# Kernel optimization log

Measured on AMD Instinct MI355X. Metric: run time of the kernel, lower is better.

## Reference

```python
import jax, jax.numpy as jnp
import numpy as np

B, S, DIM = 4, 2048, 1024
HEADS, HD = 16, DIM // 16
HIDDEN, LEVELS = 4 * DIM, 3
LN_EPS = 1e-5


def setup_inputs() -> dict:
    key = jax.random.key(0)
    ks = jax.random.split(key, 10)
    w = lambda k, shape: (jax.random.normal(k, shape, jnp.float32) * 0.02)
    return {
        "x": jax.random.normal(ks[0], (B, S, DIM), jnp.float32),
        "Wq": w(ks[1], (DIM, DIM)),
        "Wk": w(ks[2], (DIM, DIM)),
        "Wv": w(ks[3], (DIM, DIM)),
        "Wo": w(ks[4], (DIM, DIM)),
        "ln1_g": jnp.ones((DIM,), jnp.float32),
        "ln1_b": jnp.zeros((DIM,), jnp.float32),
        "ln2_g": jnp.ones((DIM,), jnp.float32),
        "ln2_b": jnp.zeros((DIM,), jnp.float32),
        "cms_w1": w(ks[5], (LEVELS, DIM, HIDDEN)),
        "cms_b1": jnp.zeros((LEVELS, HIDDEN), jnp.float32),
        "cms_w2": w(ks[6], (LEVELS, HIDDEN, DIM)),
        "cms_b2": jnp.zeros((LEVELS, DIM), jnp.float32),
    }


def _layer_norm(x, g, b):
    m = jnp.mean(x, axis=-1, keepdims=True)
    v = jnp.var(x, axis=-1, keepdims=True)
    return (x - m) * jax.lax.rsqrt(v + LN_EPS) * g + b


def _linear_attn(h, Wq, Wk, Wv, Wo):
    # h: [B, S, DIM]; feature_map(z) = elu(z) + 1 applied to Q and K
    fm = lambda z: jax.nn.elu(z) + 1.0
    Q = fm(h @ Wq).reshape(B, S, HEADS, HD)
    K = fm(h @ Wk).reshape(B, S, HEADS, HD)
    V = (h @ Wv).reshape(B, S, HEADS, HD)
    # scan over time with fast-weight memory M_t = M_{t-1} + k_t (x) v_t
    Qs = jnp.moveaxis(Q, 1, 0)  # [S, B, H, D]
    Ks = jnp.moveaxis(K, 1, 0)
    Vs = jnp.moveaxis(V, 1, 0)

    def step(carry, qkv):
        mem, ksum = carry  # [B,H,D,D], [B,H,D]
        q, k, v = qkv      # each [B,H,D]
        mem = mem + k[..., :, None] * v[..., None, :]
        ksum = ksum + k
        num = jnp.einsum('bhde,bhd->bhe', mem, q)
        den = jnp.einsum('bhd,bhd->bh', ksum, q)[..., None] + 1e-6
        return (mem, ksum), num / den

    init = (jnp.zeros((B, HEADS, HD, HD), h.dtype),
            jnp.zeros((B, HEADS, HD), h.dtype))
    _, ys = jax.lax.scan(step, init, (Qs, Ks, Vs))  # ys: [S,B,H,D]
    out = jnp.moveaxis(ys, 0, 1).reshape(B, S, DIM)
    return out @ Wo


def _cms(h, w1, b1, w2, b2):
    # Continuum Memory System: chain of LEVELS MLPs (dim->4dim->dim).
    y = h
    for l in range(LEVELS):
        y = jax.nn.gelu(y @ w1[l] + b1[l]) @ w2[l] + b2[l]
    return y


def reference(x, Wq, Wk, Wv, Wo, ln1_g, ln1_b, ln2_g, ln2_b,
              cms_w1, cms_b1, cms_w2, cms_b2):
    x = x + _linear_attn(_layer_norm(x, ln1_g, ln1_b), Wq, Wk, Wv, Wo)
    x = x + _cms(_layer_norm(x, ln2_g, ln2_b), cms_w1, cms_b1, cms_w2, cms_b2)
    return x
```

## Files before the change

kernel.cpp:

```cpp
#include <hip/hip_runtime.h>
#include <stdint.h>
#include <math.h>

#define DIM     1024
#define HID     4096
#define SEQ     2048
#define NB      4
#define NH      16
#define HD      64
#define NCHUNK  32
#define MROWS   8192
#define QSTR    3072

typedef unsigned short ushort_t;
typedef __attribute__((ext_vector_type(8))) short bf16x8;
typedef __attribute__((ext_vector_type(4))) float f32x4;

#define OFF_H    ((size_t)0)
#define OFF_Q    ((size_t)16777216)
#define OFF_P    ((size_t)67108864)
#define OFF_KS   ((size_t)100663296)
#define OFF_X1   ((size_t)101187584)
#define OFF_WQT  ((size_t)134742016)
#define OFF_WOT  ((size_t)141033472)
#define OFF_W1T  ((size_t)143130624)
#define OFF_W2T  ((size_t)168296448)
#define OFF_HIDB OFF_Q + 16777216

__device__ __forceinline__ float b2f(ushort_t u) {
    return __uint_as_float(((unsigned int)u) << 16);
}
__device__ __forceinline__ ushort_t f2b(float f) {
    unsigned int u = __float_as_uint(f);
    u += 0x7FFFu + ((u >> 16) & 1u);
    return (ushort_t)(u >> 16);
}
__device__ __forceinline__ void unpack4(uint2 u, float* f) {
    f[0] = __uint_as_float(u.x << 16);
    f[1] = __uint_as_float(u.x & 0xffff0000u);
    f[2] = __uint_as_float(u.y << 16);
    f[3] = __uint_as_float(u.y & 0xffff0000u);
}
__device__ __forceinline__ float fast_gelu(float x) {
    const float u = x * (1.5957691216057308f + 0.07135481627f * x * x);
    const float e = exp2f(-1.4426950408889634f * u);
    return x * __builtin_amdgcn_rcpf(1.0f + e);
}
__device__ __forceinline__ float fast_elu1(float x) {
    return x > 0.0f ? x + 1.0f : exp2f(1.4426950408889634f * x);
}
__device__ __forceinline__ void ldg16(const ushort_t* g, ushort_t* l) {
    __builtin_amdgcn_global_load_lds(
        (const __attribute__((address_space(1))) void*)g,
        (__attribute__((address_space(3))) void*)l, 16, 0, 0);
}

__global__ void __launch_bounds__(256)
transpose_f32_bf16(const float* __restrict__ src, ushort_t* __restrict__ dst, int R, int C)
{
    __shared__ float t[32][33];
    const int bx = blockIdx.x * 32;
    const int by = blockIdx.y * 32;
    const int tx = threadIdx.x, ty = threadIdx.y;
    #pragma unroll
    for (int i = ty; i < 32; i += 8)
        t[i][tx] = src[(size_t)(by + i) * C + bx + tx];
    __syncthreads();
    #pragma unroll
    for (int i = ty; i < 32; i += 8)
        dst[(size_t)(bx + i) * R + by + tx] = f2b(t[tx][i]);
}

__global__ void __launch_bounds__(256)
ln_fwd(const float* __restrict__ xin, const float* __restrict__ g,
       const float* __restrict__ be, ushort_t* __restrict__ out)
{
    const int row = blockIdx.x, tid = threadIdx.x;
    const float4 f = ((const float4*)(xin + (size_t)row * DIM))[tid];
    float v[4] = {f.x, f.y, f.z, f.w};
    float s  = v[0] + v[1] + v[2] + v[3];
    float ss = v[0]*v[0] + v[1]*v[1] + v[2]*v[2] + v[3]*v[3];
    #pragma unroll
    for (int off = 32; off; off >>= 1) {
        s  += __shfl_down(s, off);
        ss += __shfl_down(ss, off);
    }
    __shared__ float red[2][4];
    const int wave = tid >> 6, lane = tid & 63;
    if (lane == 0) { red[0][wave] = s; red[1][wave] = ss; }
    __syncthreads();
    s  = red[0][0] + red[0][1] + red[0][2] + red[0][3];
    ss = red[1][0] + red[1][1] + red[1][2] + red[1][3];
    const float mean = s * (1.0f / DIM);
    const float var  = ss * (1.0f / DIM) - mean * mean;
    const float rstd = rsqrtf(var + 1e-5f);
    ushort_t o[4];
    #pragma unroll
    for (int i = 0; i < 4; i++) {
        const int col = tid * 4 + i;
        o[i] = f2b((v[i] - mean) * rstd * g[col] + be[col]);
    }
    uint2 u2;
    u2.x = (unsigned int)o[0] | ((unsigned int)o[1] << 16);
    u2.y = (unsigned int)o[2] | ((unsigned int)o[3] << 16);
    *(uint2*)(out + (size_t)row * DIM + tid * 4) = u2;
}

#define ACT_NONE 0
#define ACT_ELU1 1
#define ACT_GELU 2
#define ACT_QKV  3


#define G_RD_A(BUF, FR0) \
    _Pragma("unroll") for (int _i = 0; _i < 4; ++_i) \
    _Pragma("unroll") for (int _kk = 0; _kk < 2; ++_kk) \
        af[_i][_kk] = *(const bf16x8*)(ldsb + (BUF) + aoff + (((FR0) + _i) << 11) \
                                       + (((_kk << 6) | qv16) ^ mflip))

#define G_RD_B(BUF, F) \
    _Pragma("unroll") for (int _kk = 0; _kk < 2; ++_kk) \
        bf[(F)][_kk] = *(const bf16x8*)(ldsb + (BUF) + boff + ((F) << 13) \
                                        + (((_kk << 6) | qv16) ^ mflip))

#define G_MFMA(AR, C0, CNT) \
    _Pragma("unroll") for (int _i = 0; _i < 4; ++_i) \
    _Pragma("unroll") for (int _c = 0; _c < (CNT); ++_c) \
    _Pragma("unroll") for (int _kk = 0; _kk < 2; ++_kk) \
        acc[(AR) + _i][(C0) + _c] = __builtin_amdgcn_mfma_f32_16x16x32_bf16( \
            af[_i][_kk], bf[(C0) + _c][_kk], acc[(AR) + _i][(C0) + _c], 0, 0, 0)

#define ST_A(BUFO, T, R) ldg16(pA + (size_t)(R) * K + (size_t)(T) * 64, \
    (ushort_t*)(ldsb + (BUFO) + ((R) << 7) + (tid << 4)))
#define ST_B(BUFO, T, R) ldg16(pB + (size_t)(R) * K + (size_t)(T) * 64, \
    (ushort_t*)(ldsb + (BUFO) + 32768 + ((R) << 7) + (tid << 4)))

#define G_BARW() do { \
    __builtin_amdgcn_s_barrier(); \
    asm volatile("s_waitcnt lgkmcnt(0)" ::: "memory"); \
    __builtin_amdgcn_sched_barrier(0); \
    __builtin_amdgcn_s_setprio(1); \
} while (0)

#define G_ENDP() do { \
    __builtin_amdgcn_s_setprio(0); \
    __builtin_amdgcn_s_barrier(); \
} while (0)

#define G_TILE(BUFO, TS) do { \
     \
    G_RD_A(BUFO, 0); \
    _Pragma("unroll") for (int _f = 0; _f < NF / 2; ++_f) G_RD_B(BUFO, _f); \
    G_BARW(); G_MFMA(0, 0, NF / 2); G_ENDP(); \
     \
    _Pragma("unroll") for (int _f = NF / 2; _f < NF; ++_f) G_RD_B(BUFO, _f); \
    if (more) { ST_A(BUFO, TS, 0); ST_A(BUFO, TS, 128); ST_B(BUFO, TS, 0); } \
    G_BARW(); G_MFMA(0, NF / 2, NF / 2); G_ENDP(); \
     \
    G_RD_A(BUFO, 4); \
    if (more) { \
        ST_B(BUFO, TS, 64); \
        if constexpr (NF == 4) { ST_B(BUFO, TS, 128); ST_B(BUFO, TS, 192); } \
    } \
    G_BARW(); G_MFMA(4, 0, NF / 2); G_ENDP(); \
     \
    if (more) { ST_A(BUFO, TS, 64); ST_A(BUFO, TS, 192); } \
    G_BARW(); G_MFMA(4, NF / 2, NF / 2); \
    __builtin_amdgcn_s_setprio(0); \
    if (more) asm volatile("s_waitcnt vmcnt(%0)" :: "i"(LPT) : "memory"); \
    else      asm volatile("s_waitcnt vmcnt(0)" ::: "memory"); \
    __builtin_amdgcn_s_barrier(); \
} while (0)

template<int BN_, int ACT, bool BIAS, bool RES, bool OUTF32>
__global__ void __launch_bounds__(512, 2)
gemm256(const ushort_t* __restrict__ A, const ushort_t* __restrict__ Bt,
        const float* __restrict__ bias, const float* __restrict__ resid,
        void* __restrict__ Cout, int M, int N, int K)
{
    constexpr int NF    = BN_ / 64;
    constexpr int BUFSZ = 32768 + BN_ * 128;
    constexpr int LPT   = 4 + NF;
    __shared__ __align__(16) char ldsb[2 * BUFSZ];

    const int tid  = threadIdx.x;
    const int lane = tid & 63, wave = tid >> 6;
    const int wm_idx = wave >> 2, wn_idx = wave & 3;
    const int bm = blockIdx.x * 256, bn = blockIdx.y * BN_;

    const int r0  = tid >> 3;
    const int kbs = (((tid & 7) ^ (r0 & 7)) << 4);
    const ushort_t* pA = A  + (size_t)(bm + r0) * K + (kbs >> 1);
    const ushort_t* pB = Bt + (size_t)(bn + r0) * K + (kbs >> 1);

    const int m     = lane & 15;
    const int qv16  = (lane >> 4) << 4;
    const int mflip = (m & 7) << 4;
    const int aoff  = (wm_idx * 128 + m) << 7;
    const int boff  = 32768 + ((wn_idx * 16 + m) << 7);

    f32x4  acc[8][NF] = {};
    bf16x8 af[4][2], bf[NF][2];

    const int NT    = K >> 6;
    const int niter = NT >> 1;

    ST_A(0, 0, 0); ST_A(0, 0, 64); ST_A(0, 0, 128); ST_A(0, 0, 192);
    ST_B(0, 0, 0); ST_B(0, 0, 64);
    if constexpr (NF == 4) { ST_B(0, 0, 128); ST_B(0, 0, 192); }
    ST_A(BUFSZ, 1, 0); ST_A(BUFSZ, 1, 64); ST_A(BUFSZ, 1, 128); ST_A(BUFSZ, 1, 192);
    ST_B(BUFSZ, 1, 0); ST_B(BUFSZ, 1, 64);
    if constexpr (NF == 4) { ST_B(BUFSZ, 1, 128); ST_B(BUFSZ, 1, 192); }
    asm volatile("s_waitcnt vmcnt(%0)" :: "i"(LPT) : "memory");
    __builtin_amdgcn_s_barrier();

    for (int it = 0; it < niter; ++it) {
        const int  t    = it << 1;
        const bool more = (it + 1) < niter;
        G_TILE(0,     t + 2);
        G_TILE(BUFSZ, t + 3);
    }

    const int cr   = (lane >> 4) << 2;
    const int ccol = lane & 15;
    #pragma unroll
    for (int fr = 0; fr < 8; ++fr) {
        #pragma unroll
        for (int fc = 0; fc < NF; ++fc) {
            const int gc = bn + fc * 64 + wn_idx * 16 + ccol;
            const float bv = BIAS ? bias[gc] : 0.0f;
            #pragma unroll
            for (int j = 0; j < 4; ++j) {
                const int gr = bm + wm_idx * 128 + fr * 16 + cr + j;
                float vv = acc[fr][fc][j] + bv;
                if (ACT == ACT_ELU1) vv = fast_elu1(vv);
                if (ACT == ACT_GELU) vv = fast_gelu(vv);
                if (ACT == ACT_QKV)  vv = (bn < 2048) ? fast_elu1(vv) : vv;
                const size_t oidx = (size_t)gr * N + gc;
                if (RES) vv += resid[oidx];
                if (OUTF32) ((float*)Cout)[oidx] = vv;
                else        ((ushort_t*)Cout)[oidx] = f2b(vv);
            }
        }
    }
    (void)M;
}

__global__ void __launch_bounds__(256)
attn_phase1(const ushort_t* __restrict__ qkv,
            float* __restrict__ P, float* __restrict__ Ksum)
{
    const int c = blockIdx.x, h = blockIdx.y, b = blockIdx.z;
    __shared__ ushort_t Ks[64][68], Vs[64][68];
    const int tid = threadIdx.x;
    const size_t rowbase = (size_t)b * SEQ + c * 64;
    #pragma unroll
    for (int i = 0; i < 4; i++) {
        const int lin = tid + 256 * i;
        const int t = lin >> 4, d4 = (lin & 15) * 4;
        const size_t gidx = (rowbase + t) * QSTR + h * HD + d4;
        *(uint2*)&Ks[t][d4] = *(const uint2*)(qkv + 1024 + gidx);
        *(uint2*)&Vs[t][d4] = *(const uint2*)(qkv + 2048 + gidx);
    }
    __syncthreads();
    const int d0 = (tid >> 4) * 4, e0 = (tid & 15) * 4;
    float acc[4][4] = {};
    for (int t = 0; t < 64; t++) {
        float kf[4], vf[4];
        unpack4(*(const uint2*)&Ks[t][d0], kf);
        unpack4(*(const uint2*)&Vs[t][e0], vf);
        #pragma unroll
        for (int i = 0; i < 4; i++)
            #pragma unroll
            for (int j = 0; j < 4; j++)
                acc[i][j] += kf[i] * vf[j];
    }
    const size_t pbase = (((size_t)b * NH + h) * NCHUNK + c) * 4096;
    #pragma unroll
    for (int i = 0; i < 4; i++) {
        float4 o; o.x = acc[i][0]; o.y = acc[i][1]; o.z = acc[i][2]; o.w = acc[i][3];
        *(float4*)(P + pbase + (size_t)(d0 + i) * 64 + e0) = o;
    }
    if (tid < 64) {
        float a = 0.0f;
        for (int t = 0; t < 64; t++) a += b2f(Ks[t][tid]);
        Ksum[(((size_t)b * NH + h) * NCHUNK + c) * 64 + tid] = a;
    }
}

__global__ void __launch_bounds__(256)
attn_prefix(float* __restrict__ P, float* __restrict__ Ksum)
{
    const int bh = blockIdx.y;
    const int e  = blockIdx.x * 256 + threadIdx.x;
    const size_t base = (size_t)bh * NCHUNK * 4096 + e;
    float acc = 0.0f;
    #pragma unroll
    for (int c = 0; c < NCHUNK; c++) {
        const float t = P[base + (size_t)c * 4096];
        P[base + (size_t)c * 4096] = acc;
        acc += t;
    }
    if (blockIdx.x == 0 && threadIdx.x < 64) {
        const size_t kb = (size_t)bh * NCHUNK * 64 + threadIdx.x;
        float a = 0.0f;
        #pragma unroll
        for (int c = 0; c < NCHUNK; c++) {
            const float t = Ksum[kb + c * 64];
            Ksum[kb + c * 64] = a;
            a += t;
        }
    }
}

__global__ void __launch_bounds__(256)
attn_phase2(const ushort_t* __restrict__ qkv, const float* __restrict__ P,
            const float* __restrict__ Ksum, ushort_t* __restrict__ Out)
{
    const int c = blockIdx.x, h = blockIdx.y, b = blockIdx.z;
    const int tid = threadIdx.x;
    __shared__ ushort_t Qs[64][68], KsB[64][68], VsB[64][68];
    __shared__ float S[64][68];
    __shared__ float Mp[64][64];
    __shared__ float kp[64];
    __shared__ float partial[4][64];
    const size_t rowbase = (size_t)b * SEQ + c * 64;
    const size_t pbase = (((size_t)b * NH + h) * NCHUNK + c) * 4096;
    #pragma unroll
    for (int i = 0; i < 4; i++) {
        const int lin = tid + 256 * i;
        const int t = lin >> 4, d4 = (lin & 15) * 4;
        const size_t gidx = (rowbase + t) * QSTR + h * HD + d4;
        *(uint2*)&Qs[t][d4]  = *(const uint2*)(qkv + gidx);
        *(uint2*)&KsB[t][d4] = *(const uint2*)(qkv + 1024 + gidx);
        *(uint2*)&VsB[t][d4] = *(const uint2*)(qkv + 2048 + gidx);
        *(float4*)&Mp[t][d4] = *(const float4*)(P + pbase + lin * 4);
    }
    if (tid < 64) kp[tid] = Ksum[(((size_t)b * NH + h) * NCHUNK + c) * 64 + tid];
    __syncthreads();

    const int t0 = (tid >> 4) * 4;
    const int c0 = (tid & 15) * 4;

    {
        float accS[4][4] = {};
        for (int d4 = 0; d4 < 64; d4 += 4) {
            float qf[4][4], kf[4][4];
            #pragma unroll
            for (int i = 0; i < 4; i++) {
                unpack4(*(const uint2*)&Qs[t0 + i][d4], qf[i]);
                unpack4(*(const uint2*)&KsB[c0 + i][d4], kf[i]);
            }
            #pragma unroll
            for (int i = 0; i < 4; i++)
                #pragma unroll
                for (int j = 0; j < 4; j++)
                    #pragma unroll
                    for (int dd = 0; dd < 4; dd++)
                        accS[i][j] += qf[i][dd] * kf[j][dd];
        }
        #pragma unroll
        for (int i = 0; i < 4; i++) {
            float4 sv;
            sv.x = (c0 + 0 <= t0 + i) ? accS[i][0] : 0.0f;
            sv.y = (c0 + 1 <= t0 + i) ? accS[i][1] : 0.0f;
            sv.z = (c0 + 2 <= t0 + i) ? accS[i][2] : 0.0f;
            sv.w = (c0 + 3 <= t0 + i) ? accS[i][3] : 0.0f;
            *(float4*)&S[t0 + i][c0] = sv;
        }
    }
    __syncthreads();

    {
        const int t = tid & 63, q = tid >> 6;
        const int base = q * 16;
        float a = 0.0f;
        #pragma unroll
        for (int ii = 0; ii < 16; ii++) a += S[t][base + ii];
        #pragma unroll
        for (int d = 0; d < 16; d++) a += b2f(Qs[t][base + d]) * kp[base + d];
        partial[q][t] = a;
    }
    __syncthreads();

    float acc[4][4] = {};
    for (int ii = 0; ii < 64; ii++) {
        float vf[4];
        unpack4(*(const uint2*)&VsB[ii][c0], vf);
        #pragma unroll
        for (int i = 0; i < 4; i++) {
            const float s = S[t0 + i][ii];
            #pragma unroll
            for (int j = 0; j < 4; j++) acc[i][j] += s * vf[j];
        }
    }
    for (int d = 0; d < 64; d++) {
        const float4 mp = *(const float4*)&Mp[d][c0];
        #pragma unroll
        for (int i = 0; i < 4; i++) {
            const float qv = b2f(Qs[t0 + i][d]);
            acc[i][0] += qv * mp.x; acc[i][1] += qv * mp.y;
            acc[i][2] += qv * mp.z; acc[i][3] += qv * mp.w;
        }
    }
    #pragma unroll
    for (int i = 0; i < 4; i++) {
        const float dent = partial[0][t0 + i] + partial[1][t0 + i] +
                           partial[2][t0 + i] + partial[3][t0 + i] + 1e-6f;
        const float r = 1.0f / dent;
        ushort_t o[4];
        #pragma unroll
        for (int j = 0; j < 4; j++) o[j] = f2b(acc[i][j] * r);
        uint2 u2;
        u2.x = (unsigned int)o[0] | ((unsigned int)o[1] << 16);
        u2.y = (unsigned int)o[2] | ((unsigned int)o[3] << 16);
        *(uint2*)(Out + (rowbase + t0 + i) * DIM + h * HD + c0) = u2;
    }
}

extern "C" void kernel_launch(void* const* d_in, const int* in_sizes, int n_in,
                              void* d_out, int out_size, void* d_ws, size_t ws_size,
                              hipStream_t stream)
{
    const float* x      = (const float*)d_in[0];
    const float* Wq     = (const float*)d_in[1];
    const float* Wk     = (const float*)d_in[2];
    const float* Wv     = (const float*)d_in[3];
    const float* Wo     = (const float*)d_in[4];
    const float* ln1g   = (const float*)d_in[5];
    const float* ln1b   = (const float*)d_in[6];
    const float* ln2g   = (const float*)d_in[7];
    const float* ln2b   = (const float*)d_in[8];
    const float* cw1    = (const float*)d_in[9];
    const float* cb1    = (const float*)d_in[10];
    const float* cw2    = (const float*)d_in[11];
    const float* cb2    = (const float*)d_in[12];

    char* ws = (char*)d_ws;
    ushort_t* h     = (ushort_t*)(ws + OFF_H);
    ushort_t* qkv   = (ushort_t*)(ws + OFF_Q);
    float*    Pb    = (float*)(ws + OFF_P);
    float*    ksb   = (float*)(ws + OFF_KS);
    float*    x1    = (float*)(ws + OFF_X1);
    ushort_t* wqkvt = (ushort_t*)(ws + OFF_WQT);
    ushort_t* wot   = (ushort_t*)(ws + OFF_WOT);
    ushort_t* w1t   = (ushort_t*)(ws + OFF_W1T);
    ushort_t* w2t   = (ushort_t*)(ws + OFF_W2T);
    ushort_t* hid   = (ushort_t*)(ws + OFF_HIDB);
    float*    outp  = (float*)d_out;

    const dim3 tb(32, 8);
    transpose_f32_bf16<<<dim3(32, 32), tb, 0, stream>>>(Wq, wqkvt,                   DIM, DIM);
    transpose_f32_bf16<<<dim3(32, 32), tb, 0, stream>>>(Wk, wqkvt + 1024 * 1024,     DIM, DIM);
    transpose_f32_bf16<<<dim3(32, 32), tb, 0, stream>>>(Wv, wqkvt + 2 * 1024 * 1024, DIM, DIM);
    transpose_f32_bf16<<<dim3(32, 32), tb, 0, stream>>>(Wo, wot, DIM, DIM);
    for (int l = 0; l < 3; l++) {
        transpose_f32_bf16<<<dim3(128, 32), tb, 0, stream>>>(cw1 + (size_t)l * DIM * HID,
                                                             w1t + (size_t)l * HID * DIM, DIM, HID);
        transpose_f32_bf16<<<dim3(32, 128), tb, 0, stream>>>(cw2 + (size_t)l * HID * DIM,
                                                             w2t + (size_t)l * DIM * HID, HID, DIM);
    }

    ln_fwd<<<MROWS, 256, 0, stream>>>(x, ln1g, ln1b, h);

    gemm256<128, ACT_QKV, false, false, false><<<dim3(32, 24), 512, 0, stream>>>(
        h, wqkvt, nullptr, nullptr, qkv, MROWS, QSTR, DIM);

    attn_phase1<<<dim3(NCHUNK, NH, NB), 256, 0, stream>>>(qkv, Pb, ksb);
    attn_prefix<<<dim3(16, 64), 256, 0, stream>>>(Pb, ksb);
    attn_phase2<<<dim3(NCHUNK, NH, NB), 256, 0, stream>>>(qkv, Pb, ksb, h);

    gemm256<128, ACT_NONE, false, true, true><<<dim3(32, 8), 512, 0, stream>>>(
        h, wot, nullptr, x, x1, MROWS, DIM, DIM);

    ln_fwd<<<MROWS, 256, 0, stream>>>(x1, ln2g, ln2b, h);

    const ushort_t* cur = h;
    for (int l = 0; l < 3; l++) {
        gemm256<256, ACT_GELU, true, false, false><<<dim3(32, 16), 512, 0, stream>>>(
            cur, w1t + (size_t)l * HID * DIM, cb1 + (size_t)l * HID, nullptr, hid, MROWS, HID, DIM);
        if (l < 2) {
            gemm256<128, ACT_NONE, true, false, false><<<dim3(32, 8), 512, 0, stream>>>(
                hid, w2t + (size_t)l * DIM * HID, cb2 + (size_t)l * DIM, nullptr, h, MROWS, DIM, HID);
            cur = h;
        } else {
            gemm256<128, ACT_NONE, true, true, true><<<dim3(32, 8), 512, 0, stream>>>(
                hid, w2t + (size_t)l * DIM * HID, cb2 + (size_t)l * DIM, x1, outp, MROWS, DIM, HID);
        }
    }
    (void)in_sizes; (void)n_in; (void)out_size; (void)ws_size;
}
```

Before: 892.5 us.

## Double-buffer GEMM register fragments and prefetch the next tile from LDS

The GEMM main loop now keeps two sets of A and B register fragments (low and high halves). It loads the next tile's first fragments from LDS during the last MFMA phase of the current tile, which removes the per-phase lgkmcnt waits before the MFMAs. The CMS W1 GEMM also switches from 256-wide to 128-wide N tiles with twice as many blocks. The aim is to overlap LDS reads with matrix math and improve occupancy or balance. The cost is more fragment registers and lower reuse per block for W1. The NF==4 path no longer issues all of its B-tile stores, so it is only safe because no 256-wide launch remains.

```diff
diff --git a/kernel.cpp b/kernel.cpp
--- a/kernel.cpp
+++ b/kernel.cpp
@@ -112,64 +112,56 @@
 #define ACT_QKV  3
 
 
-#define G_RD_A(BUF, FR0) \
+#define RD_AF(DST, BUFO, FR0) \
     _Pragma("unroll") for (int _i = 0; _i < 4; ++_i) \
     _Pragma("unroll") for (int _kk = 0; _kk < 2; ++_kk) \
-        af[_i][_kk] = *(const bf16x8*)(ldsb + (BUF) + aoff + (((FR0) + _i) << 11) \
-                                       + (((_kk << 6) | qv16) ^ mflip))
-
-#define G_RD_B(BUF, F) \
+        DST[_i][_kk] = *(const bf16x8*)(ldsb + (BUFO) + aoff + (((FR0) + _i) << 11) \
+                                        + (((_kk << 6) | qv16) ^ mflip))
+
+#define RD_BF(DST, BUFO, F0) \
+    _Pragma("unroll") for (int _c = 0; _c < NH2; ++_c) \
     _Pragma("unroll") for (int _kk = 0; _kk < 2; ++_kk) \
-        bf[(F)][_kk] = *(const bf16x8*)(ldsb + (BUF) + boff + ((F) << 13) \
+        DST[_c][_kk] = *(const bf16x8*)(ldsb + (BUFO) + boff + (((F0) + _c) << 13) \
                                         + (((_kk << 6) | qv16) ^ mflip))
 
-#define G_MFMA(AR, C0, CNT) \
+#define G_MM(AR, C0, AF, BF) \
     _Pragma("unroll") for (int _i = 0; _i < 4; ++_i) \
-    _Pragma("unroll") for (int _c = 0; _c < (CNT); ++_c) \
+    _Pragma("unroll") for (int _c = 0; _c < NH2; ++_c) \
     _Pragma("unroll") for (int _kk = 0; _kk < 2; ++_kk) \
         acc[(AR) + _i][(C0) + _c] = __builtin_amdgcn_mfma_f32_16x16x32_bf16( \
-            af[_i][_kk], bf[(C0) + _c][_kk], acc[(AR) + _i][(C0) + _c], 0, 0, 0)
+            AF[_i][_kk], BF[_c][_kk], acc[(AR) + _i][(C0) + _c], 0, 0, 0)
 
 #define ST_A(BUFO, T, R) ldg16(pA + (size_t)(R) * K + (size_t)(T) * 64, \
     (ushort_t*)(ldsb + (BUFO) + ((R) << 7) + (tid << 4)))
 #define ST_B(BUFO, T, R) ldg16(pB + (size_t)(R) * K + (size_t)(T) * 64, \
     (ushort_t*)(ldsb + (BUFO) + 32768 + ((R) << 7) + (tid << 4)))
 
-#define G_BARW() do { \
-    __builtin_amdgcn_s_barrier(); \
-    asm volatile("s_waitcnt lgkmcnt(0)" ::: "memory"); \
-    __builtin_amdgcn_sched_barrier(0); \
-    __builtin_amdgcn_s_setprio(1); \
-} while (0)
-
-#define G_ENDP() do { \
+#define G_PHE() do { \
     __builtin_amdgcn_s_setprio(0); \
     __builtin_amdgcn_s_barrier(); \
+    __builtin_amdgcn_sched_barrier(0); \
 } while (0)
 
-#define G_TILE(BUFO, TS) do { \
+#define G_TILE(BUFO, NBUFO, TS, MRD, MST) do { \
      \
-    G_RD_A(BUFO, 0); \
-    _Pragma("unroll") for (int _f = 0; _f < NF / 2; ++_f) G_RD_B(BUFO, _f); \
-    G_BARW(); G_MFMA(0, 0, NF / 2); G_ENDP(); \
+    RD_BF(bfh, BUFO, NH2); \
+    __builtin_amdgcn_s_setprio(1); G_MM(0, 0, afl, bfl); G_PHE(); \
      \
-    _Pragma("unroll") for (int _f = NF / 2; _f < NF; ++_f) G_RD_B(BUFO, _f); \
-    if (more) { ST_A(BUFO, TS, 0); ST_A(BUFO, TS, 128); ST_B(BUFO, TS, 0); } \
-    G_BARW(); G_MFMA(0, NF / 2, NF / 2); G_ENDP(); \
+    RD_AF(afh, BUFO, 4); \
+    if (MST) { ST_A(BUFO, TS, 0); ST_A(BUFO, TS, 128); ST_B(BUFO, TS, 0); } \
+    __builtin_amdgcn_s_setprio(1); G_MM(0, NH2, afl, bfh); G_PHE(); \
      \
-    G_RD_A(BUFO, 4); \
-    if (more) { \
-        ST_B(BUFO, TS, 64); \
-        if constexpr (NF == 4) { ST_B(BUFO, TS, 128); ST_B(BUFO, TS, 192); } \
-    } \
-    G_BARW(); G_MFMA(4, 0, NF / 2); G_ENDP(); \
+    if (MST) { ST_B(BUFO, TS, 64); } \
+    __builtin_amdgcn_s_setprio(1); G_MM(4, 0, afh, bfl); \
+    __builtin_amdgcn_s_setprio(0); \
+    if (MST) asm volatile("s_waitcnt vmcnt(%0)" :: "i"(VCT) : "memory"); \
+    else     asm volatile("s_waitcnt vmcnt(0)" ::: "memory"); \
+    __builtin_amdgcn_s_barrier(); \
+    __builtin_amdgcn_sched_barrier(0); \
      \
-    if (more) { ST_A(BUFO, TS, 64); ST_A(BUFO, TS, 192); } \
-    G_BARW(); G_MFMA(4, NF / 2, NF / 2); \
-    __builtin_amdgcn_s_setprio(0); \
-    if (more) asm volatile("s_waitcnt vmcnt(%0)" :: "i"(LPT) : "memory"); \
-    else      asm volatile("s_waitcnt vmcnt(0)" ::: "memory"); \
-    __builtin_amdgcn_s_barrier(); \
+    if (MRD) { RD_AF(afl, NBUFO, 0); RD_BF(bfl, NBUFO, 0); } \
+    if (MST) { ST_A(BUFO, TS, 64); ST_A(BUFO, TS, 192); } \
+    __builtin_amdgcn_s_setprio(1); G_MM(4, NH2, afh, bfh); G_PHE(); \
 } while (0)
 
 template<int BN_, int ACT, bool BIAS, bool RES, bool OUTF32>
@@ -179,8 +171,10 @@
         void* __restrict__ Cout, int M, int N, int K)
 {
     constexpr int NF    = BN_ / 64;
+    constexpr int NH2   = NF / 2;
     constexpr int BUFSZ = 32768 + BN_ * 128;
     constexpr int LPT   = 4 + NF;
+    constexpr int VCT   = 3 + (NF == 4 ? 3 : 1);
     __shared__ __align__(16) char ldsb[2 * BUFSZ];
 
     const int tid  = threadIdx.x;
@@ -200,7 +194,7 @@
     const int boff  = 32768 + ((wn_idx * 16 + m) << 7);
 
     f32x4  acc[8][NF] = {};
-    bf16x8 af[4][2], bf[NF][2];
+    bf16x8 afl[4][2], afh[4][2], bfl[NH2][2], bfh[NH2][2];
 
     const int NT    = K >> 6;
     const int niter = NT >> 1;
@@ -213,12 +207,14 @@
     if constexpr (NF == 4) { ST_B(BUFSZ, 1, 128); ST_B(BUFSZ, 1, 192); }
     asm volatile("s_waitcnt vmcnt(%0)" :: "i"(LPT) : "memory");
     __builtin_amdgcn_s_barrier();
+    __builtin_amdgcn_sched_barrier(0);
+    RD_AF(afl, 0, 0); RD_BF(bfl, 0, 0);
 
     for (int it = 0; it < niter; ++it) {
         const int  t    = it << 1;
         const bool more = (it + 1) < niter;
-        G_TILE(0,     t + 2);
-        G_TILE(BUFSZ, t + 3);
+        G_TILE(0,     BUFSZ, t + 2, true, more);
+        G_TILE(BUFSZ, 0,     t + 3, more, more);
     }
 
     const int cr   = (lane >> 4) << 2;
@@ -477,7 +473,7 @@
 
     const ushort_t* cur = h;
     for (int l = 0; l < 3; l++) {
-        gemm256<256, ACT_GELU, true, false, false><<<dim3(32, 16), 512, 0, stream>>>(
+        gemm256<128, ACT_GELU, true, false, false><<<dim3(32, 32), 512, 0, stream>>>(
             cur, w1t + (size_t)l * HID * DIM, cb1 + (size_t)l * HID, nullptr, hid, MROWS, HID, DIM);
         if (l < 2) {
             gemm256<128, ACT_NONE, true, false, false><<<dim3(32, 8), 512, 0, stream>>>(
```

Measured after the change: 866.1 us. 3.0% less time.
